# Kernel tuning notes

Measured on AMD Instinct MI355X. Metric: run time of the kernel, lower is better.

Reference implementation:

```python
import jax, jax.numpy as jnp
import numpy as np

B, N, E = 32, 256, 300   # batch, num hyperedges, word emb size
H, K = 256, 8            # nhidden, nhead
MARGIN = 0.2


def setup_inputs() -> dict:
    key = jax.random.key(0)
    ks = jax.random.split(key, 10)
    s_in = 1.0 / np.sqrt(E)
    s_h = 1.0 / np.sqrt(H)
    s_fc = 1.0 / np.sqrt(H * K)
    return {
        'he_anchor': jax.random.normal(ks[0], (B, N, E), jnp.float32),
        'he_pos': jax.random.normal(ks[1], (B, N, E), jnp.float32),
        'he_neg': jax.random.normal(ks[2], (B, N, E), jnp.float32),
        'W_a2h': jax.random.uniform(ks[3], (H, E), jnp.float32, -s_in, s_in),
        'b_a2h': jax.random.uniform(ks[4], (H,), jnp.float32, -s_in, s_in),
        'W_c2h': jax.random.uniform(ks[5], (H, E), jnp.float32, -s_in, s_in),
        'b_c2h': jax.random.uniform(ks[6], (H,), jnp.float32, -s_in, s_in),
        'W_att': jax.random.uniform(ks[7], (K, H), jnp.float32, -s_h, s_h),
        'b_att': jax.random.uniform(ks[8], (K,), jnp.float32, -s_h, s_h),
        'W_fc': jax.random.uniform(ks[9], (1, H * K), jnp.float32, -s_fc, s_fc),
        'b_fc': jnp.zeros((1,), jnp.float32),
    }


def _score(x, y, W_a2h, b_a2h, W_c2h, b_c2h, W_att, b_att, W_fc, b_fc):
    # a2h / c2h projections, then permute to [B, H, N]
    Aa = jnp.transpose(x @ W_a2h.T + b_a2h, (0, 2, 1))  # [B,H,N]
    Ac = jnp.transpose(y @ W_c2h.T + b_c2h, (0, 2, 1))  # [B,H,M]
    # h2att applied to the outer product Aa[b,h,n]*Ac[b,h,m]; fuse into one einsum
    logits = jnp.einsum('bhn,bhm,kh->bknm', Aa, Ac, W_att) + b_att[None, :, None, None]
    b_, k_, n_, m_ = logits.shape
    att = jax.nn.softmax(logits.reshape(b_, k_, n_ * m_), axis=-1).reshape(b_, k_, n_, m_)
    # per-head bilinear aggregation: out[b,k,h] = sum_{n,m} Aa[b,h,n]*att[b,k,n,m]*Ac[b,h,m]
    t = jnp.einsum('bhn,bknm->bkhm', Aa, att)
    out = jnp.einsum('bkhm,bhm->bkh', t, Ac)
    # torch concat order is head-major: [B, K*H]
    out = out.reshape(b_, k_ * H)
    return out @ W_fc.T + b_fc  # [B,1]


def reference(he_anchor, he_pos, he_neg, W_a2h, b_a2h, W_c2h, b_c2h, W_att, b_att, W_fc, b_fc):
    score_p = _score(he_anchor, he_pos, W_a2h, b_a2h, W_c2h, b_c2h, W_att, b_att, W_fc, b_fc)
    score_n = _score(he_anchor, he_neg, W_a2h, b_a2h, W_c2h, b_c2h, W_att, b_att, W_fc, b_fc)
    loss = jnp.mean(jax.nn.relu(score_n - score_p + MARGIN))
    return loss
```

## Files before the change

kernel.cpp:

```cpp
#include <hip/hip_runtime.h>

#define BB 32
#define NN 256
#define EE 300
#define HH 256
#define KK 8
#define MARGINF 0.2f
#define EP 320

typedef __attribute__((ext_vector_type(8))) short bf16x8;
typedef __attribute__((ext_vector_type(4))) float f32x4;
typedef __attribute__((ext_vector_type(16))) float f32x16;

__device__ inline ushort f2bf(float f) {
  unsigned u = __float_as_uint(f);
  u += 0x7fffu + ((u >> 16) & 1u);
  return (ushort)(u >> 16);
}
__device__ inline float bf2f(ushort s) { return __uint_as_float(((unsigned)s) << 16); }
__device__ inline unsigned cvtpk(float lo, float hi) {
  unsigned r;
  asm("v_cvt_pk_bf16_f32 %0, %1, %2" : "=v"(r) : "v"(lo), "v"(hi));
  return r;
}

__global__ __launch_bounds__(256) void wconv_kernel(
    const float* __restrict__ Wa, const float* __restrict__ Wc,
    ushort* __restrict__ Wt, unsigned* __restrict__ counter)
{
  const int i = blockIdx.x * 256 + threadIdx.x;
  if (i == 0) counter[0] = 0u;
  const int w = i / 81920;
  int r = i - w * 81920;
  const int hb = r / 5120; r -= hb * 5120;
  const int ks = r / 512;  r -= ks * 512;
  const int l = r >> 3, j = r & 7;
  const int h = hb * 16 + (l & 15);
  const int e = ks * 32 + (l >> 4) * 8 + j;
  const float* src = w ? Wc : Wa;
  Wt[i] = (e < EE) ? f2bf(src[h * EE + e]) : (ushort)0;
}

__global__ __launch_bounds__(256, 3) void proj_kernel(
    const float* __restrict__ he_a, const float* __restrict__ he_p,
    const float* __restrict__ he_n, const ushort* __restrict__ Wt,
    const float* __restrict__ b_a2h, const float* __restrict__ b_c2h,
    ushort* __restrict__ AT)
{
  const int z = blockIdx.y;
  const int which = z >> 5;
  const int b = z & 31;
  const int nb = blockIdx.x;
  const int n0 = nb * 32;
  const int tid = threadIdx.x;
  const int wv = tid >> 6;
  const int lane = tid & 63;
  const int col = lane & 15;
  const int quad = lane >> 4;

  const float* X = (which == 0 ? he_a : which == 1 ? he_p : he_n) + (size_t)b * NN * EE;
  const ushort* W = Wt + (size_t)(which == 0 ? 0 : 1) * 81920;
  const float* bias = (which == 0 ? b_a2h : b_c2h);

  __shared__ __align__(16) ushort sX[32][328];
  __shared__ __align__(16) ushort tr[32][264];

  {
    const int row = tid >> 3, seg = tid & 7;
    const float* xr = X + (size_t)(n0 + row) * EE;
#pragma unroll
    for (int q = 0; q < 10; q++) {
      const int jj = seg + 8 * q;
      float4 xv = {0.f, 0.f, 0.f, 0.f};
      if (jj < 75) xv = *(const float4*)&xr[4 * jj];
      uint2 p; p.x = cvtpk(xv.x, xv.y); p.y = cvtpk(xv.z, xv.w);
      *(uint2*)&sX[row][4 * jj] = p;
    }
  }
  __syncthreads();

  f32x4 acc[2][4];
#pragma unroll
  for (int nf = 0; nf < 2; nf++)
#pragma unroll
    for (int mb = 0; mb < 4; mb++) acc[nf][mb] = (f32x4){0.f, 0.f, 0.f, 0.f};

#pragma unroll
  for (int ks = 0; ks < 10; ks++) {
    const int off = 32 * ks + 8 * quad;
    const bf16x8 a0 = *(const bf16x8*)&sX[col][off];
    const bf16x8 a1 = *(const bf16x8*)&sX[16 + col][off];
#pragma unroll
    for (int mb = 0; mb < 4; mb++) {
      const bf16x8 w8 = *(const bf16x8*)&W[(4 * wv + mb) * 5120 + ks * 512 + lane * 8];
      acc[0][mb] = __builtin_amdgcn_mfma_f32_16x16x32_bf16(a0, w8, acc[0][mb], 0, 0, 0);
      acc[1][mb] = __builtin_amdgcn_mfma_f32_16x16x32_bf16(a1, w8, acc[1][mb], 0, 0, 0);
    }
  }

#pragma unroll
  for (int nf = 0; nf < 2; nf++)
#pragma unroll
    for (int mb = 0; mb < 4; mb++) {
      const float bi = bias[64 * wv + 16 * mb + col];
#pragma unroll
      for (int r = 0; r < 4; r++)
        tr[16 * nf + 4 * quad + r][64 * wv + 16 * mb + col] = f2bf(acc[nf][mb][r] + bi);
    }
  __syncthreads();
  {
    ushort* dst = AT + (size_t)(which * BB + b) * (NN * HH) + (size_t)nb * 8192;
#pragma unroll
    for (int it = 0; it < 4; it++) {
      const int c = it * 256 + tid;
      const int row = c & 31, hs = (c >> 5) & 1, hb = c >> 6;
      *(uint4*)&dst[c * 8] = *(const uint4*)&tr[row][hb * 16 + hs * 8];
    }
  }
}

__global__ __launch_bounds__(256, 2) void attn_kernel(
    const ushort* __restrict__ AT, const float* __restrict__ Watt,
    const float* __restrict__ Wfc, const float* __restrict__ bfc,
    float* __restrict__ scoresK, unsigned* __restrict__ counter,
    float* __restrict__ out)
{
  const int idx = blockIdx.x;
  const int k = idx >> 6;
  const int g = idx & 63;
  const int which = g >> 5;
  const int b = g & 31;
  const int tid = threadIdx.x;
  const int wv = tid >> 6;
  const int lane = tid & 63;

  const ushort* Ta = AT + (size_t)b * (NN * HH);
  const ushort* Tc = AT + (size_t)((1 + which) * BB + b) * (NN * HH);

  __shared__ __align__(16) float wkf[256];
  __shared__ __align__(16) float wff[256];
  __shared__ float red[8];
  __shared__ unsigned isLast;

  wkf[tid] = Watt[(size_t)k * HH + tid];
  wff[tid] = Wfc[(size_t)k * HH + tid];
  __syncthreads();

  float num = 0.f, den = 0.f;

#pragma unroll 1
  for (int s = 0; s < 2; s++) {
    const int nbk = 4 * s + wv;
    bf16x8 saf[16], gaf[16];
    const ushort* abase = Ta + nbk * 8192 + lane * 8;
#pragma unroll
    for (int ks = 0; ks < 16; ks++) {
      const bf16x8 a = *(const bf16x8*)&abase[ks * 512];
      const int off = 16 * ks + 8 * (lane >> 5);
      const float4 wa = *(const float4*)&wkf[off];
      const float4 wb = *(const float4*)&wkf[off + 4];
      const float4 fa = *(const float4*)&wff[off];
      const float4 fb = *(const float4*)&wff[off + 4];
      const float w[8] = {wa.x, wa.y, wa.z, wa.w, wb.x, wb.y, wb.z, wb.w};
      const float f[8] = {fa.x, fa.y, fa.z, fa.w, fb.x, fb.y, fb.z, fb.w};
      union { bf16x8 v; unsigned u[4]; } sv, gv;
#pragma unroll
      for (int jj = 0; jj < 4; jj++) {
        const float a0 = bf2f((ushort)a[2 * jj]), a1 = bf2f((ushort)a[2 * jj + 1]);
        sv.u[jj] = cvtpk(a0 * w[2 * jj], a1 * w[2 * jj + 1]);
        gv.u[jj] = cvtpk(a0 * f[2 * jj], a1 * f[2 * jj + 1]);
      }
      saf[ks] = sv.v; gaf[ks] = gv.v;
    }

#pragma unroll 1
    for (int mc = 0; mc < 4; mc++) {
      const ushort* cb = Tc + mc * 16384 + lane * 8;
      f32x16 aS0 = {0,0,0,0,0,0,0,0,0,0,0,0,0,0,0,0};
      f32x16 aS1 = {0,0,0,0,0,0,0,0,0,0,0,0,0,0,0,0};
      f32x16 aG0 = {0,0,0,0,0,0,0,0,0,0,0,0,0,0,0,0};
      f32x16 aG1 = {0,0,0,0,0,0,0,0,0,0,0,0,0,0,0,0};
#pragma unroll
      for (int ks = 0; ks < 16; ks++) {
        const bf16x8 b0 = *(const bf16x8*)&cb[ks * 512];
        const bf16x8 b1 = *(const bf16x8*)&cb[8192 + ks * 512];
        aS0 = __builtin_amdgcn_mfma_f32_32x32x16_bf16(saf[ks], b0, aS0, 0, 0, 0);
        aG0 = __builtin_amdgcn_mfma_f32_32x32x16_bf16(gaf[ks], b0, aG0, 0, 0, 0);
        aS1 = __builtin_amdgcn_mfma_f32_32x32x16_bf16(saf[ks], b1, aS1, 0, 0, 0);
        aG1 = __builtin_amdgcn_mfma_f32_32x32x16_bf16(gaf[ks], b1, aG1, 0, 0, 0);
      }
#pragma unroll
      for (int r = 0; r < 16; r++) {
        const float p0 = __expf(aS0[r]);
        den += p0; num += p0 * aG0[r];
        const float p1 = __expf(aS1[r]);
        den += p1; num += p1 * aG1[r];
      }
    }
  }

#pragma unroll
  for (int off = 32; off >= 1; off >>= 1) {
    num += __shfl_xor(num, off);
    den += __shfl_xor(den, off);
  }
  if (lane == 0) { red[wv] = num; red[4 + wv] = den; }
  __syncthreads();
  if (tid == 0) {
    const float nt = red[0] + red[1] + red[2] + red[3];
    const float dt = red[4] + red[5] + red[6] + red[7];
    atomicExch(&scoresK[idx], nt / dt);
    __threadfence();
    isLast = (atomicAdd(counter, 1u) == 511u) ? 1u : 0u;
  }
  __syncthreads();

  if (isLast && tid < 64) {
    float s = bfc[0];
#pragma unroll
    for (int kk = 0; kk < KK; kk++)
      s += atomicAdd(&scoresK[kk * 64 + tid], 0.0f);
    const float other = __shfl(s, tid + 32);
    float v = 0.f;
    if (tid < 32) v = fmaxf(other - s + MARGINF, 0.f);
#pragma unroll
    for (int off = 32; off >= 1; off >>= 1) v += __shfl_xor(v, off);
    if (tid == 0) out[0] = v * (1.0f / 32.0f);
  }
}

extern "C" void kernel_launch(void* const* d_in, const int* in_sizes, int n_in,
                              void* d_out, int out_size, void* d_ws, size_t ws_size,
                              hipStream_t stream) {
  const float* he_a  = (const float*)d_in[0];
  const float* he_p  = (const float*)d_in[1];
  const float* he_n  = (const float*)d_in[2];
  const float* W_a2h = (const float*)d_in[3];
  const float* b_a2h = (const float*)d_in[4];
  const float* W_c2h = (const float*)d_in[5];
  const float* b_c2h = (const float*)d_in[6];
  const float* W_att = (const float*)d_in[7];
  const float* W_fc  = (const float*)d_in[9];
  const float* b_fc  = (const float*)d_in[10];

  ushort* AT = (ushort*)d_ws;
  float* scoresK = (float*)(AT + (size_t)3 * BB * NN * HH);
  ushort* Wt = (ushort*)(scoresK + 512);
  unsigned* counter = (unsigned*)(Wt + (size_t)2 * HH * EP);
  (void)ws_size; (void)in_sizes; (void)n_in; (void)out_size;

  wconv_kernel<<<640, 256, 0, stream>>>(W_a2h, W_c2h, Wt, counter);
  dim3 pg(8, 96);
  proj_kernel<<<pg, 256, 0, stream>>>(he_a, he_p, he_n, Wt, b_a2h, b_c2h, AT);
  attn_kernel<<<512, 256, 0, stream>>>(AT, W_att, W_fc, b_fc, scoresK, counter, (float*)d_out);
}
```

Measured before the change: 142.6 us.

## Stage Ac tiles in LDS with double-buffered async loads and remap blocks

```diff
diff --git a/kernel.cpp b/kernel.cpp
--- a/kernel.cpp
+++ b/kernel.cpp
@@ -22,6 +22,11 @@
   unsigned r;
   asm("v_cvt_pk_bf16_f32 %0, %1, %2" : "=v"(r) : "v"(lo), "v"(hi));
   return r;
+}
+__device__ inline void gload_lds16(const ushort* g, ushort* l) {
+  __builtin_amdgcn_global_load_lds(
+      (const __attribute__((address_space(1))) void*)g,
+      (__attribute__((address_space(3))) void*)l, 16, 0, 0);
 }
 
 __global__ __launch_bounds__(256) void wconv_kernel(
@@ -125,11 +130,14 @@
     float* __restrict__ scoresK, unsigned* __restrict__ counter,
     float* __restrict__ out)
 {
-  const int idx = blockIdx.x;
-  const int k = idx >> 6;
-  const int g = idx & 63;
-  const int which = g >> 5;
-  const int b = g & 31;
+  const int d = blockIdx.x;
+  const int x = d & 7;
+  const int j = d >> 3;
+  const int grp = x * 8 + (j & 7);
+  const int k = j >> 3;
+  const int which = grp >> 5;
+  const int b = grp & 31;
+  const int idx = k * 64 + grp;
   const int tid = threadIdx.x;
   const int wv = tid >> 6;
   const int lane = tid & 63;
@@ -137,6 +145,7 @@
   const ushort* Ta = AT + (size_t)b * (NN * HH);
   const ushort* Tc = AT + (size_t)((1 + which) * BB + b) * (NN * HH);
 
+  __shared__ __align__(16) ushort sB[2][16384];
   __shared__ __align__(16) float wkf[256];
   __shared__ __align__(16) float wff[256];
   __shared__ float red[8];
@@ -150,6 +159,12 @@
 
 #pragma unroll 1
   for (int s = 0; s < 2; s++) {
+#pragma unroll
+    for (int it = 0; it < 8; it++) {
+      const int off = it * 2048 + wv * 512;
+      gload_lds16(Tc + off + lane * 8, &sB[0][off]);
+    }
+
     const int nbk = 4 * s + wv;
     bf16x8 saf[16], gaf[16];
     const ushort* abase = Ta + nbk * 8192 + lane * 8;
@@ -172,18 +187,28 @@
       }
       saf[ks] = sv.v; gaf[ks] = gv.v;
     }
+    __syncthreads();
 
 #pragma unroll 1
     for (int mc = 0; mc < 4; mc++) {
-      const ushort* cb = Tc + mc * 16384 + lane * 8;
+      const int cur = mc & 1;
+      if (mc < 3) {
+        const ushort* src = Tc + (mc + 1) * 16384;
+#pragma unroll
+        for (int it = 0; it < 8; it++) {
+          const int off = it * 2048 + wv * 512;
+          gload_lds16(src + off + lane * 8, &sB[cur ^ 1][off]);
+        }
+      }
+
       f32x16 aS0 = {0,0,0,0,0,0,0,0,0,0,0,0,0,0,0,0};
       f32x16 aS1 = {0,0,0,0,0,0,0,0,0,0,0,0,0,0,0,0};
       f32x16 aG0 = {0,0,0,0,0,0,0,0,0,0,0,0,0,0,0,0};
       f32x16 aG1 = {0,0,0,0,0,0,0,0,0,0,0,0,0,0,0,0};
 #pragma unroll
       for (int ks = 0; ks < 16; ks++) {
-        const bf16x8 b0 = *(const bf16x8*)&cb[ks * 512];
-        const bf16x8 b1 = *(const bf16x8*)&cb[8192 + ks * 512];
+        const bf16x8 b0 = *(const bf16x8*)&sB[cur][ks * 512 + lane * 8];
+        const bf16x8 b1 = *(const bf16x8*)&sB[cur][8192 + ks * 512 + lane * 8];
         aS0 = __builtin_amdgcn_mfma_f32_32x32x16_bf16(saf[ks], b0, aS0, 0, 0, 0);
         aG0 = __builtin_amdgcn_mfma_f32_32x32x16_bf16(gaf[ks], b0, aG0, 0, 0, 0);
         aS1 = __builtin_amdgcn_mfma_f32_32x32x16_bf16(saf[ks], b1, aS1, 0, 0, 0);
@@ -196,6 +221,7 @@
         const float p1 = __expf(aS1[r]);
         den += p1; num += p1 * aG1[r];
       }
+      __syncthreads();
     }
   }
 
```

Measured after the change: 137.1 us. -3.9%, faster.
